# Kernel optimization log

Measured on AMD Instinct MI355X. Metric: run time of the kernel, lower is better.

Reference implementation:

```python
import jax, jax.numpy as jnp
import numpy as np

NUM_HEADS = 32
ROPE_BASE = 10000.0
MASK_NEG = -66504.0  # from (1 - tril) * -66504.0 in the source


def _rotate_half(x):
    d = x.shape[-1] // 2
    return jnp.concatenate([-x[..., d:], x[..., :d]], axis=-1)


def setup_inputs() -> dict:
    key = jax.random.key(0)
    k1, k2, k3, k4 = jax.random.split(key, 4)
    S, B, E = 2048, 2, 2048
    return {
        "hidden_states": jax.random.normal(k1, (S, B, E), dtype=jnp.float32) * 0.02,
        "qkv_w": jax.random.normal(k2, (E, 3 * E), dtype=jnp.float32) * 0.02,
        "qkv_b": jax.random.normal(k3, (3 * E,), dtype=jnp.float32) * 0.02,
        "out_w": jax.random.normal(k4, (E, E), dtype=jnp.float32) * 0.02,
        "out_b": jnp.zeros((E,), dtype=jnp.float32),
    }


def reference(hidden_states, qkv_w, qkv_b, out_w, out_b):
    # seq-first prompt/prefill path of IPEXTransformerAtten
    S, B, E = hidden_states.shape
    H = NUM_HEADS
    D = E // H

    # fused QKV projection (mm_qkv_out)
    qkv = jnp.einsum('sbe,ef->sbf', hidden_states, qkv_w) + qkv_b  # [S,B,3E]
    q, k, v = jnp.split(qkv, 3, axis=-1)
    q = q.reshape(S, B, H, D)
    k = k.reshape(S, B, H, D)
    v = v.reshape(S, B, H, D)

    # rotary embedding (GPT-NeoX style, full head_dim)
    inv_freq = 1.0 / (ROPE_BASE ** (jnp.arange(0, D, 2, dtype=jnp.float32) / D))
    freqs = jnp.arange(S, dtype=jnp.float32)[:, None] * inv_freq  # [S, D/2]
    emb = jnp.concatenate([freqs, freqs], axis=-1)  # [S, D]
    cos = jnp.cos(emb)[:, None, None, :].astype(hidden_states.dtype)
    sin = jnp.sin(emb)[:, None, None, :].astype(hidden_states.dtype)
    q = q * cos + _rotate_half(q) * sin
    k = k * cos + _rotate_half(k) * sin

    # scaled dot-product attention with causal mask
    scale = 1.0 / jnp.sqrt(jnp.array(D, dtype=hidden_states.dtype))
    scores = jnp.einsum('sbhd,tbhd->bhst', q, k) * scale  # [B,H,S,S]
    causal = jnp.tril(jnp.ones((S, S), dtype=scores.dtype))
    scores = scores + (1.0 - causal) * MASK_NEG
    attn = jax.nn.softmax(scores, axis=-1)
    ctx = jnp.einsum('bhst,tbhd->sbhd', attn, v).reshape(S, B, E)

    # output projection
    return jnp.einsum('sbe,ef->sbf', ctx, out_w) + out_b
```

## Files before the change

kernel.cpp:

```cpp
#include <hip/hip_runtime.h>
#include <hip/hip_bf16.h>

#define S_LEN 2048
#define BATCH 2
#define EMB   2048
#define NH    32
#define HD    64
#define M_ROWS (S_LEN * BATCH)
#define QKV_N  (3 * EMB)

typedef short bf16x8 __attribute__((ext_vector_type(8)));
typedef float f32x4  __attribute__((ext_vector_type(4)));

__device__ __forceinline__ unsigned short f2bf(float f) {
  unsigned int u = __float_as_uint(f);
  u += 0x7fffu + ((u >> 16) & 1u);
  return (unsigned short)(u >> 16);
}
__device__ __forceinline__ float bf2f(unsigned short h) {
  return __uint_as_float(((unsigned int)h) << 16);
}
__device__ __forceinline__ void async_copy16(const void* g, void* lds) {
  __builtin_amdgcn_global_load_lds(
      (const __attribute__((address_space(1))) void*)g,
      (__attribute__((address_space(3))) void*)lds, 16, 0, 0);
}

#if __has_builtin(__builtin_amdgcn_exp2f)
#define EXP2F(x) __builtin_amdgcn_exp2f(x)
#else
#define EXP2F(x) __expf((x) * 0.6931471805599453f)
#endif


__global__ __launch_bounds__(256) void cast_to_bf16(
    const float* __restrict__ in, unsigned short* __restrict__ out, int n4) {
  int i = blockIdx.x * 256 + threadIdx.x;
  if (i >= n4) return;
  float4 v = reinterpret_cast<const float4*>(in)[i];
  ushort4 o;
  o.x = f2bf(v.x); o.y = f2bf(v.y); o.z = f2bf(v.z); o.w = f2bf(v.w);
  reinterpret_cast<ushort4*>(out)[i] = o;
}

__global__ __launch_bounds__(256) void transpose_cast(
    const float* __restrict__ in, unsigned short* __restrict__ out, int R, int C) {
  __shared__ float tile[32][33];
  const int bc = blockIdx.x * 32, br = blockIdx.y * 32;
  const int tx = threadIdx.x & 31, ty = threadIdx.x >> 5;
  #pragma unroll
  for (int rr = ty; rr < 32; rr += 8)
    tile[rr][tx] = in[(size_t)(br + rr) * C + bc + tx];
  __syncthreads();
  #pragma unroll
  for (int rr = ty; rr < 32; rr += 8)
    out[(size_t)(bc + rr) * R + br + tx] = f2bf(tile[tx][rr]);
}


__global__ __launch_bounds__(256) void gemm_qkv(
    const unsigned short* __restrict__ A,
    const unsigned short* __restrict__ Wt,
    const float* __restrict__ bias,
    unsigned short* __restrict__ Qo,
    unsigned short* __restrict__ Ko,
    unsigned short* __restrict__ Vo) {
  __shared__ __align__(16) unsigned short As[128 * 64];
  __shared__ __align__(16) unsigned short Bs[128 * 64];
  const int tid = threadIdx.x;
  const int n0 = blockIdx.x * 128;
  const int m0 = blockIdx.y * 128;
  const int wave = tid >> 6, lane = tid & 63;
  const int wm = (wave >> 1) * 64, wn = (wave & 1) * 64;
  const int lm = lane & 15, lq = lane >> 4;
  const int K = 2048;

  const int srow = tid >> 3;
  const int gch  = (tid & 7) ^ (srow & 7);
  const unsigned short* Ab = A  + (size_t)(m0 + srow) * K + gch * 8;
  const unsigned short* Bb = Wt + (size_t)(n0 + srow) * K + gch * 8;

  f32x4 acc[4][4] = {};

  for (int k0 = 0; k0 < K; k0 += 64) {
    #pragma unroll
    for (int rep = 0; rep < 4; rep++) {
      async_copy16(Ab + (size_t)rep * 32 * K + k0, As + (size_t)(tid + 256 * rep) * 8);
      async_copy16(Bb + (size_t)rep * 32 * K + k0, Bs + (size_t)(tid + 256 * rep) * 8);
    }
    __syncthreads();
    #pragma unroll
    for (int ks = 0; ks < 2; ks++) {
      bf16x8 a[4], b[4];
      #pragma unroll
      for (int i = 0; i < 4; i++) {
        const int R = wm + i*16 + lm;
        a[i] = *reinterpret_cast<const bf16x8*>(
            As + (size_t)R * 64 + (((ks*4 + lq) ^ (R & 7)) * 8));
      }
      #pragma unroll
      for (int j = 0; j < 4; j++) {
        const int R = wn + j*16 + lm;
        b[j] = *reinterpret_cast<const bf16x8*>(
            Bs + (size_t)R * 64 + (((ks*4 + lq) ^ (R & 7)) * 8));
      }
      #pragma unroll
      for (int i = 0; i < 4; i++)
        #pragma unroll
        for (int j = 0; j < 4; j++)
          acc[i][j] = __builtin_amdgcn_mfma_f32_16x16x32_bf16(a[i], b[j], acc[i][j], 0, 0, 0);
    }
    __syncthreads();
  }

  const int which = n0 >> 11;
  unsigned short* dst = (which == 0) ? Qo : (which == 1) ? Ko : Vo;
  float bv[4];
  #pragma unroll
  for (int j = 0; j < 4; j++) bv[j] = bias[n0 + wn + j*16 + lm];

  if (which < 2) {
    #pragma unroll
    for (int j = 0; j < 2; j++) {
      const int n = n0 + wn + j*16 + lm;
      const int e = n & (EMB - 1), h = e >> 6, d = e & 63;
      const float invf = EXP2F((float)d * -0.4152410118609203f);
      #pragma unroll
      for (int i = 0; i < 4; i++) {
        #pragma unroll
        for (int r = 0; r < 4; r++) {
          const int m = m0 + wm + i*16 + lq*4 + r;
          const int s = m >> 1, b = m & 1;
          const float v1 = acc[i][j][r]   + bv[j];
          const float v2 = acc[i][j+2][r] + bv[j+2];
          float sn, cs;
          __sincosf((float)s * invf, &sn, &cs);
          const size_t base = (((size_t)b * NH + h) * S_LEN + s) * HD + d;
          dst[base]      = f2bf(v1 * cs - v2 * sn);
          dst[base + 32] = f2bf(v2 * cs + v1 * sn);
        }
      }
    }
  } else {
    #pragma unroll
    for (int j = 0; j < 4; j++) {
      const int n = n0 + wn + j*16 + lm;
      const int e = n & (EMB - 1), h = e >> 6, d = e & 63;
      #pragma unroll
      for (int i = 0; i < 4; i++) {
        #pragma unroll
        for (int r = 0; r < 4; r++) {
          const int m = m0 + wm + i*16 + lq*4 + r;
          const int s = m >> 1, b = m & 1;
          dst[(((size_t)b * NH + h) * S_LEN + s) * HD + d] = f2bf(acc[i][j][r] + bv[j]);
        }
      }
    }
  }
}


__global__ __launch_bounds__(256) void transpose_v(
    const unsigned short* __restrict__ V, unsigned short* __restrict__ VT) {
  __shared__ unsigned short t[64][65];
  const int bh = blockIdx.y;
  const int s0 = blockIdx.x * 64;
  const int tx = threadIdx.x & 63, ty = threadIdx.x >> 6;
  const unsigned short* src = V + ((size_t)bh * S_LEN + s0) * HD;
  #pragma unroll
  for (int r = ty; r < 64; r += 4)
    t[r][tx] = src[(size_t)r * HD + tx];
  __syncthreads();
  unsigned short* dst = VT + (size_t)bh * HD * S_LEN + s0;
  #pragma unroll
  for (int r = ty; r < 64; r += 4)
    dst[(size_t)r * S_LEN + tx] = t[tx][r];
}


__device__ __forceinline__ void attn_qblock(
    const char* __restrict__ Qb8,
    const char* __restrict__ Kb8,
    const char* __restrict__ Vb8,
    unsigned short* __restrict__ ctx,
    char* __restrict__ KsB,
    char* __restrict__ VsB,
    unsigned short* __restrict__ Pw,
    int q0, int b, int h, int tid, int wave, int lm, int lq) {
  const float C = 0.18033688011112042f;
  const int r0 = q0 + wave * 32;
  const int nt = (q0 >> 6) + 2;
  const int srow_c = r0 + lq * 4;

  const int srw = tid >> 2, sc16 = (tid & 3) * 16;

  bf16x8 qf[2][2];
  #pragma unroll
  for (int i = 0; i < 2; i++)
    #pragma unroll
    for (int ks = 0; ks < 2; ks++)
      qf[i][ks] = *reinterpret_cast<const bf16x8*>(
          Qb8 + (size_t)(r0 + i*16 + lm) * 128 + ks*64 + lq*16);

  f32x4 O[2][4] = {};
  float l[2][4] = {};

  for (int t = 0; t < nt; t++) {
    const int t0 = t * 64;
    async_copy16(Kb8 + (size_t)(t0 + srw) * 128      + sc16, KsB        + tid*16);
    async_copy16(Kb8 + (size_t)(t0 + srw) * 128 + 64 + sc16, KsB + 4096 + tid*16);
    async_copy16(Vb8 + (size_t)srw * 4096 + t0*2      + sc16, VsB        + tid*16);
    async_copy16(Vb8 + (size_t)srw * 4096 + t0*2 + 64 + sc16, VsB + 4096 + tid*16);
    __syncthreads();

    if (t0 <= r0 + 31) {
      const bool clean = (t0 + 63 <= r0);
      const int jmax  = clean ? 4 : ((r0 == t0) ? 2 : 4);
      const int kslim = clean ? 2 : ((r0 == t0) ? 1 : 2);

      f32x4 sc[2][4] = {};
      #pragma unroll
      for (int ks = 0; ks < 2; ks++) {
        bf16x8 kf[4];
        #pragma unroll
        for (int j = 0; j < 4; j++)
          if (j < jmax)
            kf[j] = *reinterpret_cast<const bf16x8*>(
                KsB + ks*4096 + (j*16 + lm)*64 + lq*16);
        #pragma unroll
        for (int i = 0; i < 2; i++)
          #pragma unroll
          for (int j = 0; j < 4; j++)
            if (j < jmax)
              sc[i][j] = __builtin_amdgcn_mfma_f32_16x16x32_bf16(qf[i][ks], kf[j], sc[i][j], 0, 0, 0);
      }

      if (clean) {
        #pragma unroll
        for (int i = 0; i < 2; i++)
          #pragma unroll
          for (int j = 0; j < 4; j++)
            #pragma unroll
            for (int r = 0; r < 4; r++) {
              const float p = EXP2F(sc[i][j][r] * C);
              l[i][r] += p;
              Pw[(i*16 + lq*4 + r) * 72 + j*16 + lm] = f2bf(p);
            }
      } else {
        #pragma unroll
        for (int i = 0; i < 2; i++)
          #pragma unroll
          for (int j = 0; j < 4; j++)
            if (j < jmax)
              #pragma unroll
              for (int r = 0; r < 4; r++) {
                const int srow = srow_c + i*16 + r;
                const int tcol = t0 + j*16 + lm;
                const float p = (tcol <= srow) ? EXP2F(sc[i][j][r] * C) : 0.0f;
                l[i][r] += p;
                Pw[(i*16 + lq*4 + r) * 72 + j*16 + lm] = f2bf(p);
              }
      }

      #pragma unroll
      for (int ks = 0; ks < 2; ks++) {
        if (ks < kslim) {
          bf16x8 pf[2], vf[4];
          #pragma unroll
          for (int i = 0; i < 2; i++)
            pf[i] = *reinterpret_cast<const bf16x8*>(Pw + (i*16 + lm)*72 + ks*32 + lq*8);
          #pragma unroll
          for (int j = 0; j < 4; j++)
            vf[j] = *reinterpret_cast<const bf16x8*>(
                VsB + ks*4096 + (j*16 + lm)*64 + lq*16);
          #pragma unroll
          for (int i = 0; i < 2; i++)
            #pragma unroll
            for (int j = 0; j < 4; j++)
              O[i][j] = __builtin_amdgcn_mfma_f32_16x16x32_bf16(pf[i], vf[j], O[i][j], 0, 0, 0);
        }
      }
    }
    __syncthreads();
  }

  #pragma unroll
  for (int i = 0; i < 2; i++) {
    #pragma unroll
    for (int r = 0; r < 4; r++) {
      float s = l[i][r];
      s += __shfl_xor(s, 1, 64);
      s += __shfl_xor(s, 2, 64);
      s += __shfl_xor(s, 4, 64);
      s += __shfl_xor(s, 8, 64);
      const float inv = 1.0f / s;
      const int srow = srow_c + i*16 + r;
      #pragma unroll
      for (int j = 0; j < 4; j++) {
        const int d = j*16 + lm;
        ctx[((size_t)srow * BATCH + b) * EMB + h*HD + d] = f2bf(O[i][j][r] * inv);
      }
    }
  }
}

__global__ __launch_bounds__(256) void attn_kernel(
    const unsigned short* __restrict__ Q,
    const unsigned short* __restrict__ K,
    const unsigned short* __restrict__ VT,
    unsigned short* __restrict__ ctx) {
  const int bh = blockIdx.x;
  const int p  = blockIdx.y;
  const int tid = threadIdx.x;
  const int wave = tid >> 6, lane = tid & 63;
  const int lm = lane & 15, lq = lane >> 4;
  const int b = bh >> 5, h = bh & 31;
  const char* Qb8 = (const char*)(Q  + (size_t)bh * S_LEN * HD);
  const char* Kb8 = (const char*)(K  + (size_t)bh * S_LEN * HD);
  const char* Vb8 = (const char*)(VT + (size_t)bh * HD * S_LEN);

  __shared__ __align__(16) unsigned short Ks[2][64][32];
  __shared__ __align__(16) unsigned short Vs[2][64][32];
  __shared__ __align__(16) unsigned short Pbuf[4][32][72];
  char* KsB = (char*)&Ks[0][0][0];
  char* VsB = (char*)&Vs[0][0][0];
  unsigned short* Pw = &Pbuf[wave][0][0];

  attn_qblock(Qb8, Kb8, Vb8, ctx, KsB, VsB, Pw, p * 128,        b, h, tid, wave, lm, lq);
  attn_qblock(Qb8, Kb8, Vb8, ctx, KsB, VsB, Pw, (15 - p) * 128, b, h, tid, wave, lm, lq);
}


__global__ __launch_bounds__(256) void gemm_out(
    const unsigned short* __restrict__ A,
    const unsigned short* __restrict__ Wt,
    const float* __restrict__ bias,
    float* __restrict__ out) {
  __shared__ __align__(16) unsigned short As[128 * 64];
  __shared__ __align__(16) unsigned short Bs[128 * 64];
  const int tid = threadIdx.x;
  const int n0 = blockIdx.x * 128;
  const int m0 = blockIdx.y * 128;
  const int wave = tid >> 6, lane = tid & 63;
  const int wm = (wave >> 1) * 64, wn = (wave & 1) * 64;
  const int lm = lane & 15, lq = lane >> 4;
  const int K = 2048;

  const int srow = tid >> 3;
  const int gch  = (tid & 7) ^ (srow & 7);
  const unsigned short* Ab = A  + (size_t)(m0 + srow) * K + gch * 8;
  const unsigned short* Bb = Wt + (size_t)(n0 + srow) * K + gch * 8;

  f32x4 acc[4][4] = {};

  for (int k0 = 0; k0 < K; k0 += 64) {
    #pragma unroll
    for (int rep = 0; rep < 4; rep++) {
      async_copy16(Ab + (size_t)rep * 32 * K + k0, As + (size_t)(tid + 256 * rep) * 8);
      async_copy16(Bb + (size_t)rep * 32 * K + k0, Bs + (size_t)(tid + 256 * rep) * 8);
    }
    __syncthreads();
    #pragma unroll
    for (int ks = 0; ks < 2; ks++) {
      bf16x8 a[4], b[4];
      #pragma unroll
      for (int i = 0; i < 4; i++) {
        const int R = wm + i*16 + lm;
        a[i] = *reinterpret_cast<const bf16x8*>(
            As + (size_t)R * 64 + (((ks*4 + lq) ^ (R & 7)) * 8));
      }
      #pragma unroll
      for (int j = 0; j < 4; j++) {
        const int R = wn + j*16 + lm;
        b[j] = *reinterpret_cast<const bf16x8*>(
            Bs + (size_t)R * 64 + (((ks*4 + lq) ^ (R & 7)) * 8));
      }
      #pragma unroll
      for (int i = 0; i < 4; i++)
        #pragma unroll
        for (int j = 0; j < 4; j++)
          acc[i][j] = __builtin_amdgcn_mfma_f32_16x16x32_bf16(a[i], b[j], acc[i][j], 0, 0, 0);
    }
    __syncthreads();
  }

  #pragma unroll
  for (int j = 0; j < 4; j++) {
    const int n = n0 + wn + j*16 + lm;
    const float bv = bias[n];
    #pragma unroll
    for (int i = 0; i < 4; i++) {
      #pragma unroll
      for (int r = 0; r < 4; r++) {
        const int m = m0 + wm + i*16 + lq*4 + r;
        out[(size_t)m * EMB + n] = acc[i][j][r] + bv;
      }
    }
  }
}


extern "C" void kernel_launch(void* const* d_in, const int* in_sizes, int n_in,
                              void* d_out, int out_size, void* d_ws, size_t ws_size,
                              hipStream_t stream) {
  const float* hidden = (const float*)d_in[0];
  const float* qkv_w  = (const float*)d_in[1];
  const float* qkv_b  = (const float*)d_in[2];
  const float* out_w  = (const float*)d_in[3];
  const float* out_b  = (const float*)d_in[4];
  float* out = (float*)d_out;

  unsigned short* ws = (unsigned short*)d_ws;
  unsigned short* hbf   = ws;
  unsigned short* qkvwT = hbf   + (size_t)M_ROWS * EMB;
  unsigned short* outwT = qkvwT + (size_t)QKV_N * EMB;
  unsigned short* Qb    = outwT + (size_t)EMB * EMB;
  unsigned short* Kb    = Qb    + (size_t)64 * S_LEN * HD;
  unsigned short* Vb    = Kb    + (size_t)64 * S_LEN * HD;
  unsigned short* VTb   = Vb    + (size_t)64 * S_LEN * HD;
  unsigned short* ctx   = VTb   + (size_t)64 * S_LEN * HD;

  cast_to_bf16<<<(M_ROWS * EMB / 4) / 256, 256, 0, stream>>>(hidden, hbf, M_ROWS * EMB / 4);
  transpose_cast<<<dim3(QKV_N / 32, EMB / 32), 256, 0, stream>>>(qkv_w, qkvwT, EMB, QKV_N);
  transpose_cast<<<dim3(EMB / 32, EMB / 32), 256, 0, stream>>>(out_w, outwT, EMB, EMB);

  gemm_qkv<<<dim3(QKV_N / 128, M_ROWS / 128), 256, 0, stream>>>(hbf, qkvwT, qkv_b, Qb, Kb, Vb);

  transpose_v<<<dim3(S_LEN / 64, 64), 256, 0, stream>>>(Vb, VTb);

  attn_kernel<<<dim3(64, 8), 256, 0, stream>>>(Qb, Kb, VTb, ctx);

  gemm_out<<<dim3(EMB / 128, M_ROWS / 128), 256, 0, stream>>>(ctx, outwT, out_b, out);
}
```

Measured before the change: 380.6 us.

## Fuse paired query blocks into one K/V sweep with double-buffered LDS tiles

The attention kernel used to walk the K/V sequence twice, once per query block (p and 15-p). It now walks it once, and each loaded K/V tile is used by both query blocks, so global K/V traffic and barriers are roughly halved. The K/V LDS tiles are also double-buffered: the next tile's async copy starts before the current tile is computed, hiding load latency. In exchange the kernel holds twice the Q fragments, O accumulators and row sums in registers and uses twice the K/V LDS, which may reduce occupancy.

```diff
diff --git a/kernel.cpp b/kernel.cpp
--- a/kernel.cpp
+++ b/kernel.cpp
@@ -178,132 +178,6 @@
 }
 
 
-__device__ __forceinline__ void attn_qblock(
-    const char* __restrict__ Qb8,
-    const char* __restrict__ Kb8,
-    const char* __restrict__ Vb8,
-    unsigned short* __restrict__ ctx,
-    char* __restrict__ KsB,
-    char* __restrict__ VsB,
-    unsigned short* __restrict__ Pw,
-    int q0, int b, int h, int tid, int wave, int lm, int lq) {
-  const float C = 0.18033688011112042f;
-  const int r0 = q0 + wave * 32;
-  const int nt = (q0 >> 6) + 2;
-  const int srow_c = r0 + lq * 4;
-
-  const int srw = tid >> 2, sc16 = (tid & 3) * 16;
-
-  bf16x8 qf[2][2];
-  #pragma unroll
-  for (int i = 0; i < 2; i++)
-    #pragma unroll
-    for (int ks = 0; ks < 2; ks++)
-      qf[i][ks] = *reinterpret_cast<const bf16x8*>(
-          Qb8 + (size_t)(r0 + i*16 + lm) * 128 + ks*64 + lq*16);
-
-  f32x4 O[2][4] = {};
-  float l[2][4] = {};
-
-  for (int t = 0; t < nt; t++) {
-    const int t0 = t * 64;
-    async_copy16(Kb8 + (size_t)(t0 + srw) * 128      + sc16, KsB        + tid*16);
-    async_copy16(Kb8 + (size_t)(t0 + srw) * 128 + 64 + sc16, KsB + 4096 + tid*16);
-    async_copy16(Vb8 + (size_t)srw * 4096 + t0*2      + sc16, VsB        + tid*16);
-    async_copy16(Vb8 + (size_t)srw * 4096 + t0*2 + 64 + sc16, VsB + 4096 + tid*16);
-    __syncthreads();
-
-    if (t0 <= r0 + 31) {
-      const bool clean = (t0 + 63 <= r0);
-      const int jmax  = clean ? 4 : ((r0 == t0) ? 2 : 4);
-      const int kslim = clean ? 2 : ((r0 == t0) ? 1 : 2);
-
-      f32x4 sc[2][4] = {};
-      #pragma unroll
-      for (int ks = 0; ks < 2; ks++) {
-        bf16x8 kf[4];
-        #pragma unroll
-        for (int j = 0; j < 4; j++)
-          if (j < jmax)
-            kf[j] = *reinterpret_cast<const bf16x8*>(
-                KsB + ks*4096 + (j*16 + lm)*64 + lq*16);
-        #pragma unroll
-        for (int i = 0; i < 2; i++)
-          #pragma unroll
-          for (int j = 0; j < 4; j++)
-            if (j < jmax)
-              sc[i][j] = __builtin_amdgcn_mfma_f32_16x16x32_bf16(qf[i][ks], kf[j], sc[i][j], 0, 0, 0);
-      }
-
-      if (clean) {
-        #pragma unroll
-        for (int i = 0; i < 2; i++)
-          #pragma unroll
-          for (int j = 0; j < 4; j++)
-            #pragma unroll
-            for (int r = 0; r < 4; r++) {
-              const float p = EXP2F(sc[i][j][r] * C);
-              l[i][r] += p;
-              Pw[(i*16 + lq*4 + r) * 72 + j*16 + lm] = f2bf(p);
-            }
-      } else {
-        #pragma unroll
-        for (int i = 0; i < 2; i++)
-          #pragma unroll
-          for (int j = 0; j < 4; j++)
-            if (j < jmax)
-              #pragma unroll
-              for (int r = 0; r < 4; r++) {
-                const int srow = srow_c + i*16 + r;
-                const int tcol = t0 + j*16 + lm;
-                const float p = (tcol <= srow) ? EXP2F(sc[i][j][r] * C) : 0.0f;
-                l[i][r] += p;
-                Pw[(i*16 + lq*4 + r) * 72 + j*16 + lm] = f2bf(p);
-              }
-      }
-
-      #pragma unroll
-      for (int ks = 0; ks < 2; ks++) {
-        if (ks < kslim) {
-          bf16x8 pf[2], vf[4];
-          #pragma unroll
-          for (int i = 0; i < 2; i++)
-            pf[i] = *reinterpret_cast<const bf16x8*>(Pw + (i*16 + lm)*72 + ks*32 + lq*8);
-          #pragma unroll
-          for (int j = 0; j < 4; j++)
-            vf[j] = *reinterpret_cast<const bf16x8*>(
-                VsB + ks*4096 + (j*16 + lm)*64 + lq*16);
-          #pragma unroll
-          for (int i = 0; i < 2; i++)
-            #pragma unroll
-            for (int j = 0; j < 4; j++)
-              O[i][j] = __builtin_amdgcn_mfma_f32_16x16x32_bf16(pf[i], vf[j], O[i][j], 0, 0, 0);
-        }
-      }
-    }
-    __syncthreads();
-  }
-
-  #pragma unroll
-  for (int i = 0; i < 2; i++) {
-    #pragma unroll
-    for (int r = 0; r < 4; r++) {
-      float s = l[i][r];
-      s += __shfl_xor(s, 1, 64);
-      s += __shfl_xor(s, 2, 64);
-      s += __shfl_xor(s, 4, 64);
-      s += __shfl_xor(s, 8, 64);
-      const float inv = 1.0f / s;
-      const int srow = srow_c + i*16 + r;
-      #pragma unroll
-      for (int j = 0; j < 4; j++) {
-        const int d = j*16 + lm;
-        ctx[((size_t)srow * BATCH + b) * EMB + h*HD + d] = f2bf(O[i][j][r] * inv);
-      }
-    }
-  }
-}
-
 __global__ __launch_bounds__(256) void attn_kernel(
     const unsigned short* __restrict__ Q,
     const unsigned short* __restrict__ K,
@@ -319,15 +193,160 @@
   const char* Kb8 = (const char*)(K  + (size_t)bh * S_LEN * HD);
   const char* Vb8 = (const char*)(VT + (size_t)bh * HD * S_LEN);
 
-  __shared__ __align__(16) unsigned short Ks[2][64][32];
-  __shared__ __align__(16) unsigned short Vs[2][64][32];
+  __shared__ __align__(16) unsigned short Ks[2][2][64][32];
+  __shared__ __align__(16) unsigned short Vs[2][2][64][32];
   __shared__ __align__(16) unsigned short Pbuf[4][32][72];
-  char* KsB = (char*)&Ks[0][0][0];
-  char* VsB = (char*)&Vs[0][0][0];
   unsigned short* Pw = &Pbuf[wave][0][0];
 
-  attn_qblock(Qb8, Kb8, Vb8, ctx, KsB, VsB, Pw, p * 128,        b, h, tid, wave, lm, lq);
-  attn_qblock(Qb8, Kb8, Vb8, ctx, KsB, VsB, Pw, (15 - p) * 128, b, h, tid, wave, lm, lq);
+  const float C = 0.18033688011112042f;
+  const int q0A = p * 128, q0B = (15 - p) * 128;
+  const int r0A = q0A + wave * 32, r0B = q0B + wave * 32;
+  const int nt = (q0B >> 6) + 2;
+
+  const int srw = tid >> 2, sc16 = (tid & 3) * 16;
+
+  bf16x8 qf[2][2][2];
+  #pragma unroll
+  for (int s = 0; s < 2; s++) {
+    const int rr = (s == 0) ? r0A : r0B;
+    #pragma unroll
+    for (int i = 0; i < 2; i++)
+      #pragma unroll
+      for (int ks = 0; ks < 2; ks++)
+        qf[s][i][ks] = *reinterpret_cast<const bf16x8*>(
+            Qb8 + (size_t)(rr + i*16 + lm) * 128 + ks*64 + lq*16);
+  }
+
+  f32x4 O[2][2][4] = {};
+  float l[2][2][4] = {};
+
+  {
+    char* kd = (char*)&Ks[0][0][0][0];
+    char* vd = (char*)&Vs[0][0][0][0];
+    async_copy16(Kb8 + (size_t)srw * 128      + sc16, kd        + tid*16);
+    async_copy16(Kb8 + (size_t)srw * 128 + 64 + sc16, kd + 4096 + tid*16);
+    async_copy16(Vb8 + (size_t)srw * 4096      + sc16, vd        + tid*16);
+    async_copy16(Vb8 + (size_t)srw * 4096 + 64 + sc16, vd + 4096 + tid*16);
+  }
+  __syncthreads();
+
+  for (int t = 0; t < nt; t++) {
+    const int t0 = t * 64;
+    const int buf = t & 1;
+
+    if (t + 1 < nt) {
+      const int t1 = t0 + 64;
+      char* kd = (char*)&Ks[buf ^ 1][0][0][0];
+      char* vd = (char*)&Vs[buf ^ 1][0][0][0];
+      async_copy16(Kb8 + (size_t)(t1 + srw) * 128      + sc16, kd        + tid*16);
+      async_copy16(Kb8 + (size_t)(t1 + srw) * 128 + 64 + sc16, kd + 4096 + tid*16);
+      async_copy16(Vb8 + (size_t)srw * 4096 + t1*2      + sc16, vd        + tid*16);
+      async_copy16(Vb8 + (size_t)srw * 4096 + t1*2 + 64 + sc16, vd + 4096 + tid*16);
+    }
+
+    const char* KsB = (const char*)&Ks[buf][0][0][0];
+    const char* VsB = (const char*)&Vs[buf][0][0][0];
+
+    #pragma unroll
+    for (int s = 0; s < 2; s++) {
+      const int rr = (s == 0) ? r0A : r0B;
+      if (t0 <= rr + 31) {
+        const bool clean = (t0 + 63 <= rr);
+        const int jmax  = clean ? 4 : ((rr == t0) ? 2 : 4);
+        const int kslim = clean ? 2 : ((rr == t0) ? 1 : 2);
+        const int srow_c = rr + lq * 4;
+
+        f32x4 sc[2][4] = {};
+        #pragma unroll
+        for (int ks = 0; ks < 2; ks++) {
+          bf16x8 kf[4];
+          #pragma unroll
+          for (int j = 0; j < 4; j++)
+            if (j < jmax)
+              kf[j] = *reinterpret_cast<const bf16x8*>(
+                  KsB + ks*4096 + (j*16 + lm)*64 + lq*16);
+          #pragma unroll
+          for (int i = 0; i < 2; i++)
+            #pragma unroll
+            for (int j = 0; j < 4; j++)
+              if (j < jmax)
+                sc[i][j] = __builtin_amdgcn_mfma_f32_16x16x32_bf16(
+                    qf[s][i][ks], kf[j], sc[i][j], 0, 0, 0);
+        }
+
+        if (clean) {
+          #pragma unroll
+          for (int i = 0; i < 2; i++)
+            #pragma unroll
+            for (int j = 0; j < 4; j++)
+              #pragma unroll
+              for (int r = 0; r < 4; r++) {
+                const float pe = EXP2F(sc[i][j][r] * C);
+                l[s][i][r] += pe;
+                Pw[(i*16 + lq*4 + r) * 72 + j*16 + lm] = f2bf(pe);
+              }
+        } else {
+          #pragma unroll
+          for (int i = 0; i < 2; i++)
+            #pragma unroll
+            for (int j = 0; j < 4; j++)
+              if (j < jmax)
+                #pragma unroll
+                for (int r = 0; r < 4; r++) {
+                  const int srow = srow_c + i*16 + r;
+                  const int tcol = t0 + j*16 + lm;
+                  const float pe = (tcol <= srow) ? EXP2F(sc[i][j][r] * C) : 0.0f;
+                  l[s][i][r] += pe;
+                  Pw[(i*16 + lq*4 + r) * 72 + j*16 + lm] = f2bf(pe);
+                }
+        }
+
+        #pragma unroll
+        for (int ks = 0; ks < 2; ks++) {
+          if (ks < kslim) {
+            bf16x8 pf[2], vf[4];
+            #pragma unroll
+            for (int i = 0; i < 2; i++)
+              pf[i] = *reinterpret_cast<const bf16x8*>(Pw + (i*16 + lm)*72 + ks*32 + lq*8);
+            #pragma unroll
+            for (int j = 0; j < 4; j++)
+              vf[j] = *reinterpret_cast<const bf16x8*>(
+                  VsB + ks*4096 + (j*16 + lm)*64 + lq*16);
+            #pragma unroll
+            for (int i = 0; i < 2; i++)
+              #pragma unroll
+              for (int j = 0; j < 4; j++)
+                O[s][i][j] = __builtin_amdgcn_mfma_f32_16x16x32_bf16(
+                    pf[i], vf[j], O[s][i][j], 0, 0, 0);
+          }
+        }
+      }
+    }
+    __syncthreads();
+  }
+
+  #pragma unroll
+  for (int s = 0; s < 2; s++) {
+    const int rr = (s == 0) ? r0A : r0B;
+    #pragma unroll
+    for (int i = 0; i < 2; i++) {
+      #pragma unroll
+      for (int r = 0; r < 4; r++) {
+        float sum = l[s][i][r];
+        sum += __shfl_xor(sum, 1, 64);
+        sum += __shfl_xor(sum, 2, 64);
+        sum += __shfl_xor(sum, 4, 64);
+        sum += __shfl_xor(sum, 8, 64);
+        const float inv = 1.0f / sum;
+        const int srow = rr + lq*4 + i*16 + r;
+        #pragma unroll
+        for (int j = 0; j < 4; j++) {
+          const int d = j*16 + lm;
+          ctx[((size_t)srow * BATCH + b) * EMB + h*HD + d] = f2bf(O[s][i][j][r] * inv);
+        }
+      }
+    }
+  }
 }
 
 
```

Result: faster. 368.1 us (-3.3%).
